# Optimization experiments

Measured on AMD Instinct MI355X. Metric: run time of the kernel, lower is better.

The kernel has to match this reference:

```python
import jax, jax.numpy as jnp
import numpy as np

B, N, C = 4, 2048, 1024
H = 16
D = C // H
FF = 4096
EPS = 1e-6


def _layernorm(x, g, b):
    mu = jnp.mean(x, axis=-1, keepdims=True)
    var = jnp.mean(jnp.square(x - mu), axis=-1, keepdims=True)
    return (x - mu) * jax.lax.rsqrt(var + EPS) * g + b


def setup_inputs() -> dict:
    key = jax.random.key(0)
    ks = jax.random.split(key, 8)
    s = 0.02
    x = jax.random.normal(ks[0], (B, N, C), dtype=jnp.float32)
    mask = jnp.tril(jnp.ones((N, N), dtype=bool))[None, None]  # causal [1,1,N,N]
    return {
        "x": x,
        "mask": mask,
        "qkv_w": jax.random.normal(ks[1], (3 * C, C), jnp.float32) * s,
        "qkv_b": jnp.zeros((3 * C,), jnp.float32),
        "proj_w": jax.random.normal(ks[2], (C, C), jnp.float32) * s,
        "proj_b": jnp.zeros((C,), jnp.float32),
        "ln1_g": jnp.ones((C,), jnp.float32),
        "ln1_b": jnp.zeros((C,), jnp.float32),
        "ln2_g": jnp.ones((C,), jnp.float32),
        "ln2_b": jnp.zeros((C,), jnp.float32),
        "w1": jax.random.normal(ks[3], (FF, C), jnp.float32) * s,
        "w2": jax.random.normal(ks[4], (C, FF), jnp.float32) * s,
        "w3": jax.random.normal(ks[5], (FF, C), jnp.float32) * s,
    }


def reference(x, mask, qkv_w, qkv_b, proj_w, proj_b, ln1_g, ln1_b, ln2_g, ln2_b, w1, w2, w3):
    # --- attention sub-block (pre-norm) ---
    h = _layernorm(x, ln1_g, ln1_b)
    qkv = h @ qkv_w.T + qkv_b                      # [B,N,3C]
    qkv = qkv.reshape(B, N, 3, H, D).transpose(2, 0, 3, 1, 4)  # [3,B,H,N,D]
    q, k, v = qkv[0], qkv[1], qkv[2]
    scale = D ** -0.5
    attn = jnp.einsum("bhnd,bhmd->bhnm", q, k) * scale
    attn = jnp.where(mask, attn, -jnp.inf)
    attn = jax.nn.softmax(attn, axis=-1)
    o = jnp.einsum("bhnm,bhmd->bhnd", attn, v)
    o = o.transpose(0, 2, 1, 3).reshape(B, N, C)
    o = o @ proj_w.T + proj_b
    x = x + o  # dropout is identity in eval mode
    # --- SwiGLU MLP sub-block (pre-norm) ---
    h = _layernorm(x, ln2_g, ln2_b)
    m = (jax.nn.silu(h @ w1.T) * (h @ w3.T)) @ w2.T
    return x + m
```

## Files before the change

kernel.cpp:

```cpp
#include <hip/hip_runtime.h>
#include <hip/hip_bf16.h>
#include <stdint.h>

#define NB   4
#define NSEQ 2048
#define NC   1024
#define NH   16
#define ND   64
#define NFF  4096
#define NM   (NB*NSEQ)

typedef __attribute__((ext_vector_type(8))) short short8v;
typedef __attribute__((ext_vector_type(4))) short short4v;
typedef __attribute__((ext_vector_type(4))) float f32x4;

#define GPTR(p) ((const __attribute__((address_space(1))) void*)(p))
#define LPTR(p) ((__attribute__((address_space(3))) void*)(p))

__device__ __forceinline__ short f2bf(float f){
  unsigned u = __builtin_bit_cast(unsigned, f);
  u += 0x7fffu + ((u >> 16) & 1u);
  return (short)(u >> 16);
}
__device__ __forceinline__ float bf2f(short h){
  unsigned u = ((unsigned)(unsigned short)h) << 16;
  return __builtin_bit_cast(float, u);
}
__device__ __forceinline__ f32x4 mfma16x32(short8v a, short8v b, f32x4 c){
  return __builtin_amdgcn_mfma_f32_16x16x32_bf16(a, b, c, 0, 0, 0);
}
__device__ __forceinline__ f32x4 mfma16x16(short4v a, short4v b, f32x4 c){
  return __builtin_amdgcn_mfma_f32_16x16x16bf16_1k(a, b, c, 0, 0, 0);
}
__device__ __forceinline__ short4v pack4bf(f32x4 v){
  __hip_bfloat162 a = __float22bfloat162_rn(float2{v[0], v[1]});
  __hip_bfloat162 b = __float22bfloat162_rn(float2{v[2], v[3]});
  short4v r;
  __builtin_memcpy(&r, &a, 4);
  __builtin_memcpy(((char*)&r) + 4, &b, 4);
  return r;
}

__global__ __launch_bounds__(256) void cvt_kernel(const float* __restrict__ w,
                                                  short* __restrict__ o, int n){
  int i = (blockIdx.x * 256 + threadIdx.x) * 4;
  if (i >= n) return;
  float4 v = *(const float4*)(w + i);
  short4v r = { f2bf(v.x), f2bf(v.y), f2bf(v.z), f2bf(v.w) };
  *(short4v*)(o + i) = r;
}

__global__ __launch_bounds__(256) void ln_kernel(const float* __restrict__ x,
                                                 const float* __restrict__ g,
                                                 const float* __restrict__ bta,
                                                 short* __restrict__ out){
  int row = blockIdx.x;
  int tid = threadIdx.x;
  int lane = tid & 63, w = tid >> 6;
  const float4* xr = (const float4*)(x + (size_t)row * NC);
  float4 v = xr[tid];
  float s1 = v.x + v.y + v.z + v.w;
  float s2 = v.x*v.x + v.y*v.y + v.z*v.z + v.w*v.w;
  #pragma unroll
  for (int off = 32; off; off >>= 1){
    s1 += __shfl_xor(s1, off);
    s2 += __shfl_xor(s2, off);
  }
  __shared__ float red[8];
  if (lane == 0){ red[w] = s1; red[4 + w] = s2; }
  __syncthreads();
  s1 = red[0] + red[1] + red[2] + red[3];
  s2 = red[4] + red[5] + red[6] + red[7];
  float mean = s1 * (1.0f / NC);
  float var  = s2 * (1.0f / NC) - mean * mean;
  float inv  = rsqrtf(var + 1e-6f);
  float4 gv = ((const float4*)g)[tid];
  float4 bv = ((const float4*)bta)[tid];
  short4v o = { f2bf((v.x - mean) * inv * gv.x + bv.x),
                f2bf((v.y - mean) * inv * gv.y + bv.y),
                f2bf((v.z - mean) * inv * gv.z + bv.z),
                f2bf((v.w - mean) * inv * gv.w + bv.w) };
  *(short4v*)(out + (size_t)row * NC + tid * 4) = o;
}

template<bool HAS_BIAS, bool HAS_RES, bool OUT_BF16, bool QKV_V>
__global__ __launch_bounds__(256, 2) void gemm_bt(const short* __restrict__ A,
                                                  const short* __restrict__ Bm,
                                                  const float* __restrict__ bias,
                                                  const float* __restrict__ res,
                                                  void* __restrict__ outp,
                                                  short* __restrict__ vt,
                                                  int Nc, int K){
  __shared__ short Al[128 * 32];
  __shared__ short Bl[128 * 32];
  int tid = threadIdx.x;
  int m0 = blockIdx.y * 128, n0 = blockIdx.x * 128;
  const short* Ag = A + (size_t)m0 * K;
  const short* Bg = Bm + (size_t)n0 * K;
  int lr = tid >> 2, lc = (tid & 3) * 8;
  int lane = tid & 63, wid = tid >> 6;
  int wm = (wid >> 1) * 64, wn = (wid & 1) * 64;
  int qd = lane >> 4, l15 = lane & 15;

  f32x4 acc[4][4] = {};

  for (int k0 = 0; k0 < K; k0 += 32){
    __syncthreads();
    #pragma unroll
    for (int i = 0; i < 2; i++){
      int r = i * 64 + lr;
      __builtin_amdgcn_global_load_lds(GPTR(Ag + (size_t)r * K + k0 + lc),
                                       LPTR(&Al[r * 32 + lc]), 16, 0, 0);
      __builtin_amdgcn_global_load_lds(GPTR(Bg + (size_t)r * K + k0 + lc),
                                       LPTR(&Bl[r * 32 + lc]), 16, 0, 0);
    }
    __syncthreads();
    short8v a[4], b[4];
    #pragma unroll
    for (int t = 0; t < 4; t++)
      a[t] = *(const short8v*)&Al[(wm + t * 16 + l15) * 32 + qd * 8];
    #pragma unroll
    for (int t = 0; t < 4; t++)
      b[t] = *(const short8v*)&Bl[(wn + t * 16 + l15) * 32 + qd * 8];
    #pragma unroll
    for (int i = 0; i < 4; i++)
      #pragma unroll
      for (int j = 0; j < 4; j++)
        acc[i][j] = mfma16x32(a[i], b[j], acc[i][j]);
  }

  #pragma unroll
  for (int ti = 0; ti < 4; ti++){
    #pragma unroll
    for (int tj = 0; tj < 4; tj++){
      int col = n0 + wn + tj * 16 + l15;
      float bv = HAS_BIAS ? bias[col] : 0.0f;
      #pragma unroll
      for (int r = 0; r < 4; r++){
        int row = m0 + wm + ti * 16 + qd * 4 + r;
        float v = acc[ti][tj][r] + bv;
        if (QKV_V && col >= 2048){
          int hh = (col - 2048) >> 6, dd = col & 63;
          int bb = row >> 11, nn = row & 2047;
          vt[(((size_t)(bb * 16 + hh) * 64 + dd) << 11) + nn] = f2bf(v);
        } else {
          size_t idx = (size_t)row * Nc + col;
          if (HAS_RES) v += res[idx];
          if (OUT_BF16) ((short*)outp)[idx] = f2bf(v);
          else          ((float*)outp)[idx] = v;
        }
      }
    }
  }
}

__global__ __launch_bounds__(256) void attn_kernel(const short* __restrict__ qkvb,
                                                   const short* __restrict__ vt,
                                                   short* __restrict__ outb){
  const float QSCALE = 0.125f * 1.44269504f;
  int bh = blockIdx.x;
  int qb = 15 - blockIdx.y;
  int b = bh >> 4, h = bh & 15;
  int tid = threadIdx.x;
  int lane = tid & 63, wid = tid >> 6;
  int qd = lane >> 4, l15 = lane & 15;
  int qs = qb * 128 + wid * 32;

  const short* qbase = qkvb + (size_t)b * NSEQ * 3072 + h * 64;
  const short* kbase = qbase + 1024;
  const short* vtb   = vt + ((size_t)bh << 17);

  __shared__ short Kl[2][64 * 64];
  __shared__ short Vl[2][64 * 64];

  short8v qf[2][2];
  #pragma unroll
  for (int g = 0; g < 2; g++)
    #pragma unroll
    for (int kc = 0; kc < 2; kc++){
      short8v q = *(const short8v*)(qbase + (size_t)(qs + g * 16 + l15) * 3072
                                    + kc * 32 + qd * 8);
      short8v r;
      #pragma unroll
      for (int j = 0; j < 8; j++) r[j] = f2bf(bf2f(q[j]) * QSCALE);
      qf[g][kc] = r;
    }

  float l_i[2] = { 0.f, 0.f };
  f32x4 o[2][4];
  #pragma unroll
  for (int g = 0; g < 2; g++)
    #pragma unroll
    for (int t = 0; t < 4; t++)
      o[g][t] = (f32x4){0.f, 0.f, 0.f, 0.f};

  int nkt_blk = 2 * qb + 2;
  int itmax   = (qs + 31) >> 6;

  auto STAGE = [&](int bufi, int k0){
    #pragma unroll
    for (int i = 0; i < 2; i++){
      int cg = (wid * 2 + i) * 64 + lane;
      int r  = cg >> 3, c = cg & 7;
      int sc = (c ^ (r & 7)) << 3;
      __builtin_amdgcn_global_load_lds(GPTR(kbase + (size_t)(k0 + r) * 3072 + sc),
                                       LPTR(&Kl[bufi][cg * 8]), 16, 0, 0);
      __builtin_amdgcn_global_load_lds(GPTR(vtb + ((size_t)r << 11) + k0 + sc),
                                       LPTR(&Vl[bufi][cg * 8]), 16, 0, 0);
    }
  };

  STAGE(0, 0);
  __syncthreads();
  int cur = 0;

  for (int it = 0; it < nkt_blk; ++it){
    if (it + 1 < nkt_blk) STAGE(cur ^ 1, (it + 1) * 64);

    if (it <= itmax){
      int k0 = it * 64;
      short8v kf[4][2];
      #pragma unroll
      for (int kt = 0; kt < 4; kt++)
        #pragma unroll
        for (int kc = 0; kc < 2; kc++){
          int r = kt * 16 + l15;
          kf[kt][kc] = *(const short8v*)
              &Kl[cur][r * 64 + (((kc * 4 + qd) ^ (r & 7)) << 3)];
        }
      short4v vf[4][4];
      #pragma unroll
      for (int t = 0; t < 4; t++)
        #pragma unroll
        for (int ks = 0; ks < 4; ks++){
          int r = t * 16 + l15;
          vf[t][ks] = *(const short4v*)
              &Vl[cur][r * 64 + (((ks * 2 + (qd >> 1)) ^ (r & 7)) << 3)
                       + ((qd & 1) << 2)];
        }

      f32x4 s[2][4];
      #pragma unroll
      for (int g = 0; g < 2; g++)
        #pragma unroll
        for (int kt = 0; kt < 4; kt++){
          f32x4 z = (f32x4){0.f, 0.f, 0.f, 0.f};
          z = mfma16x32(kf[kt][0], qf[g][0], z);
          s[g][kt] = mfma16x32(kf[kt][1], qf[g][1], z);
        }

      if (it == itmax){
        #pragma unroll
        for (int g = 0; g < 2; g++){
          int qg = qs + g * 16 + l15;
          #pragma unroll
          for (int kt = 0; kt < 4; kt++)
            #pragma unroll
            for (int r = 0; r < 4; r++){
              int kg = k0 + kt * 16 + qd * 4 + r;
              s[g][kt][r] = (kg <= qg) ? s[g][kt][r] : -1e30f;
            }
        }
      }

      short4v pb[2][4];
      #pragma unroll
      for (int g = 0; g < 2; g++){
        #pragma unroll
        for (int kt = 0; kt < 4; kt++){
          f32x4 p;
          #pragma unroll
          for (int r = 0; r < 4; r++){
            float pv = exp2f(fminf(s[g][kt][r], 24.0f));
            p[r] = pv;
            l_i[g] += pv;
          }
          pb[g][kt] = pack4bf(p);
        }
      }

      #pragma unroll
      for (int g = 0; g < 2; g++)
        #pragma unroll
        for (int t = 0; t < 4; t++)
          #pragma unroll
          for (int ks = 0; ks < 4; ks++)
            o[g][t] = mfma16x16(vf[t][ks], pb[g][ks], o[g][t]);
    }

    __syncthreads();
    cur ^= 1;
  }

  #pragma unroll
  for (int g = 0; g < 2; g++){
    float l = l_i[g];
    l += __shfl_xor(l, 16);
    l += __shfl_xor(l, 32);
    float inv_l = 1.0f / l;
    int q = qs + g * 16 + l15;
    size_t rowbase = ((size_t)(b * NSEQ + q)) * NC + h * 64;
    #pragma unroll
    for (int t = 0; t < 4; t++){
      f32x4 v = { o[g][t][0] * inv_l, o[g][t][1] * inv_l,
                  o[g][t][2] * inv_l, o[g][t][3] * inv_l };
      *(short4v*)(outb + rowbase + t * 16 + qd * 4) = pack4bf(v);
    }
  }
}

__global__ __launch_bounds__(256) void silu_mul_kernel(short* __restrict__ a,
                                                       const short* __restrict__ c, int n){
  int i = (blockIdx.x * 256 + threadIdx.x) * 8;
  if (i >= n) return;
  short8v av = *(const short8v*)(a + i);
  short8v cv = *(const short8v*)(c + i);
  short8v r;
  #pragma unroll
  for (int j = 0; j < 8; j++){
    float x = bf2f(av[j]);
    float y = bf2f(cv[j]);
    float s = x / (1.0f + __expf(-x));
    r[j] = f2bf(s * y);
  }
  *(short8v*)(a + i) = r;
}

extern "C" void kernel_launch(void* const* d_in, const int* in_sizes, int n_in,
                              void* d_out, int out_size, void* d_ws, size_t ws_size,
                              hipStream_t stream){
  const float* x      = (const float*)d_in[0];
  const float* qkv_w  = (const float*)d_in[2];
  const float* qkv_b  = (const float*)d_in[3];
  const float* proj_w = (const float*)d_in[4];
  const float* proj_b = (const float*)d_in[5];
  const float* ln1_g  = (const float*)d_in[6];
  const float* ln1_b  = (const float*)d_in[7];
  const float* ln2_g  = (const float*)d_in[8];
  const float* ln2_b  = (const float*)d_in[9];
  const float* w1     = (const float*)d_in[10];
  const float* w2     = (const float*)d_in[11];
  const float* w3     = (const float*)d_in[12];
  float* out = (float*)d_out;

  short* wqkv  = (short*)d_ws;
  short* wproj = wqkv  + (size_t)3072 * 1024;
  short* w1b   = wproj + (size_t)1024 * 1024;
  short* w3b   = w1b   + (size_t)4096 * 1024;
  short* w2b   = w3b   + (size_t)4096 * 1024;
  short* hb    = w2b   + (size_t)4096 * 1024;
  short* qkvb  = hb    + (size_t)NM * NC;
  short* attnb = qkvb  + (size_t)NM * 3072;
  short* ff3b  = attnb + (size_t)NM * NC;
  float* x1    = (float*)(ff3b + (size_t)NM * NFF);
  short* ff1b  = qkvb;
  short* vtb   = ff3b;

  cvt_kernel<<<3072 * 1024 / 1024, 256, 0, stream>>>(qkv_w, wqkv, 3072 * 1024);
  cvt_kernel<<<1024, 256, 0, stream>>>(proj_w, wproj, 1024 * 1024);
  cvt_kernel<<<4096, 256, 0, stream>>>(w1, w1b, 4096 * 1024);
  cvt_kernel<<<4096, 256, 0, stream>>>(w3, w3b, 4096 * 1024);
  cvt_kernel<<<4096, 256, 0, stream>>>(w2, w2b, 4096 * 1024);

  ln_kernel<<<NM, 256, 0, stream>>>(x, ln1_g, ln1_b, hb);
  gemm_bt<true, false, true, true><<<dim3(3072 / 128, NM / 128), 256, 0, stream>>>(
      hb, wqkv, qkv_b, nullptr, qkvb, vtb, 3072, 1024);
  attn_kernel<<<dim3(NB * NH, NSEQ / 128), 256, 0, stream>>>(qkvb, vtb, attnb);
  gemm_bt<true, true, false, false><<<dim3(1024 / 128, NM / 128), 256, 0, stream>>>(
      attnb, wproj, proj_b, x, x1, nullptr, 1024, 1024);
  ln_kernel<<<NM, 256, 0, stream>>>(x1, ln2_g, ln2_b, hb);
  gemm_bt<false, false, true, false><<<dim3(4096 / 128, NM / 128), 256, 0, stream>>>(
      hb, w1b, nullptr, nullptr, ff1b, nullptr, 4096, 1024);
  gemm_bt<false, false, true, false><<<dim3(4096 / 128, NM / 128), 256, 0, stream>>>(
      hb, w3b, nullptr, nullptr, ff3b, nullptr, 4096, 1024);
  silu_mul_kernel<<<(NM * NFF) / (256 * 8), 256, 0, stream>>>(ff1b, ff3b, NM * NFF);
  gemm_bt<false, true, false, false><<<dim3(1024 / 128, NM / 128), 256, 0, stream>>>(
      ff1b, w2b, nullptr, x1, out, nullptr, 1024, 4096);
}
```

Baseline: 676.8 us.

## Fuse w1/w3 GEMMs with SiLU-mul epilogue and add XCD-aware block swizzle

Measured after the change: 629.3 us. 7.0% less time.

```diff
diff --git a/kernel.cpp b/kernel.cpp
--- a/kernel.cpp
+++ b/kernel.cpp
@@ -39,6 +39,12 @@
   __builtin_memcpy(&r, &a, 4);
   __builtin_memcpy(((char*)&r) + 4, &b, 4);
   return r;
+}
+
+__device__ __forceinline__ int xcd_swizzle(){
+  int nwg = gridDim.x * gridDim.y;
+  int wg  = blockIdx.y * gridDim.x + blockIdx.x;
+  return (wg & 7) * (nwg >> 3) + (wg >> 3);
 }
 
 __global__ __launch_bounds__(256) void cvt_kernel(const float* __restrict__ w,
@@ -94,7 +100,8 @@
   __shared__ short Al[128 * 32];
   __shared__ short Bl[128 * 32];
   int tid = threadIdx.x;
-  int m0 = blockIdx.y * 128, n0 = blockIdx.x * 128;
+  int swz = xcd_swizzle();
+  int m0 = (swz / gridDim.x) * 128, n0 = (swz % gridDim.x) * 128;
   const short* Ag = A + (size_t)m0 * K;
   const short* Bg = Bm + (size_t)n0 * K;
   int lr = tid >> 2, lc = (tid & 3) * 8;
@@ -154,6 +161,74 @@
   }
 }
 
+__global__ __launch_bounds__(256, 2) void gemm_ff13(const short* __restrict__ A,
+                                                    const short* __restrict__ B1m,
+                                                    const short* __restrict__ B3m,
+                                                    short* __restrict__ outp){
+  __shared__ short Al [128 * 32];
+  __shared__ short B1l[128 * 32];
+  __shared__ short B3l[128 * 32];
+  int tid = threadIdx.x;
+  int swz = xcd_swizzle();
+  int m0 = (swz / gridDim.x) * 128, n0 = (swz % gridDim.x) * 128;
+  const short* Ag  = A   + (size_t)m0 * NC;
+  const short* B1g = B1m + (size_t)n0 * NC;
+  const short* B3g = B3m + (size_t)n0 * NC;
+  int lr = tid >> 2, lc = (tid & 3) * 8;
+  int lane = tid & 63, wid = tid >> 6;
+  int wm = (wid >> 1) * 64, wn = (wid & 1) * 64;
+  int qd = lane >> 4, l15 = lane & 15;
+
+  f32x4 acc1[4][4] = {}, acc3[4][4] = {};
+
+  for (int k0 = 0; k0 < NC; k0 += 32){
+    __syncthreads();
+    #pragma unroll
+    for (int i = 0; i < 2; i++){
+      int r = i * 64 + lr;
+      __builtin_amdgcn_global_load_lds(GPTR(Ag + (size_t)r * NC + k0 + lc),
+                                       LPTR(&Al[r * 32 + lc]), 16, 0, 0);
+      __builtin_amdgcn_global_load_lds(GPTR(B1g + (size_t)r * NC + k0 + lc),
+                                       LPTR(&B1l[r * 32 + lc]), 16, 0, 0);
+      __builtin_amdgcn_global_load_lds(GPTR(B3g + (size_t)r * NC + k0 + lc),
+                                       LPTR(&B3l[r * 32 + lc]), 16, 0, 0);
+    }
+    __syncthreads();
+    short8v a[4], b1[4], b3[4];
+    #pragma unroll
+    for (int t = 0; t < 4; t++)
+      a[t] = *(const short8v*)&Al[(wm + t * 16 + l15) * 32 + qd * 8];
+    #pragma unroll
+    for (int t = 0; t < 4; t++){
+      b1[t] = *(const short8v*)&B1l[(wn + t * 16 + l15) * 32 + qd * 8];
+      b3[t] = *(const short8v*)&B3l[(wn + t * 16 + l15) * 32 + qd * 8];
+    }
+    #pragma unroll
+    for (int i = 0; i < 4; i++)
+      #pragma unroll
+      for (int j = 0; j < 4; j++){
+        acc1[i][j] = mfma16x32(a[i], b1[j], acc1[i][j]);
+        acc3[i][j] = mfma16x32(a[i], b3[j], acc3[i][j]);
+      }
+  }
+
+  #pragma unroll
+  for (int ti = 0; ti < 4; ti++){
+    #pragma unroll
+    for (int tj = 0; tj < 4; tj++){
+      int col = n0 + wn + tj * 16 + l15;
+      #pragma unroll
+      for (int r = 0; r < 4; r++){
+        int row = m0 + wm + ti * 16 + qd * 4 + r;
+        float v1 = acc1[ti][tj][r];
+        float v3 = acc3[ti][tj][r];
+        float s = v1 / (1.0f + __expf(-v1)) * v3;
+        outp[(size_t)row * NFF + col] = f2bf(s);
+      }
+    }
+  }
+}
+
 __global__ __launch_bounds__(256) void attn_kernel(const short* __restrict__ qkvb,
                                                    const short* __restrict__ vt,
                                                    short* __restrict__ outb){
@@ -307,23 +382,6 @@
       *(short4v*)(outb + rowbase + t * 16 + qd * 4) = pack4bf(v);
     }
   }
-}
-
-__global__ __launch_bounds__(256) void silu_mul_kernel(short* __restrict__ a,
-                                                       const short* __restrict__ c, int n){
-  int i = (blockIdx.x * 256 + threadIdx.x) * 8;
-  if (i >= n) return;
-  short8v av = *(const short8v*)(a + i);
-  short8v cv = *(const short8v*)(c + i);
-  short8v r;
-  #pragma unroll
-  for (int j = 0; j < 8; j++){
-    float x = bf2f(av[j]);
-    float y = bf2f(cv[j]);
-    float s = x / (1.0f + __expf(-x));
-    r[j] = f2bf(s * y);
-  }
-  *(short8v*)(a + i) = r;
 }
 
 extern "C" void kernel_launch(void* const* d_in, const int* in_sizes, int n_in,
@@ -369,11 +427,7 @@
   gemm_bt<true, true, false, false><<<dim3(1024 / 128, NM / 128), 256, 0, stream>>>(
       attnb, wproj, proj_b, x, x1, nullptr, 1024, 1024);
   ln_kernel<<<NM, 256, 0, stream>>>(x1, ln2_g, ln2_b, hb);
-  gemm_bt<false, false, true, false><<<dim3(4096 / 128, NM / 128), 256, 0, stream>>>(
-      hb, w1b, nullptr, nullptr, ff1b, nullptr, 4096, 1024);
-  gemm_bt<false, false, true, false><<<dim3(4096 / 128, NM / 128), 256, 0, stream>>>(
-      hb, w3b, nullptr, nullptr, ff3b, nullptr, 4096, 1024);
-  silu_mul_kernel<<<(NM * NFF) / (256 * 8), 256, 0, stream>>>(ff1b, ff3b, NM * NFF);
+  gemm_ff13<<<dim3(4096 / 128, NM / 128), 256, 0, stream>>>(hb, w1b, w3b, ff1b);
   gemm_bt<false, true, false, false><<<dim3(1024 / 128, NM / 128), 256, 0, stream>>>(
       ff1b, w2b, nullptr, x1, out, nullptr, 1024, 4096);
 }
```
